# Kernel optimization log

Hardware: AMD Instinct MI355X
Metric: run time of the kernel (lower is better)

## Reference

```python
import jax, jax.numpy as jnp
import numpy as np

CHEB_K = 3

def avwgcn(x, E, W_pool, b_pool):
    # x: [B,N,Cin], E: [N,e], W_pool: [e,K,Cin,Cout], b_pool: [e,Cout]
    N = E.shape[0]
    A = jax.nn.softmax(jax.nn.relu(E @ E.T), axis=1)          # adaptive adjacency [N,N]
    supports = [jnp.eye(N, dtype=x.dtype), A]
    for _ in range(2, CHEB_K):
        supports.append(2.0 * (A @ supports[-1]) - supports[-2])
    S = jnp.stack(supports)                                    # [K,N,N]
    W = jnp.einsum('ne,ekio->nkio', E, W_pool)                 # per-node weights
    b = E @ b_pool                                             # [N,Cout]
    xg = jnp.einsum('knm,bmi->bnki', S, x)                     # Chebyshev graph conv
    return jnp.einsum('bnki,nkio->bno', xg, W) + b


def setup_inputs() -> dict:
    key = jax.random.key(0)
    ks = jax.random.split(key, 7)
    B, N, Din, Dout, E_DIM = 64, 1024, 64, 64, 16
    C = Din + Dout
    return {
        'x': jax.random.normal(ks[0], (B, N, Din), dtype=jnp.float32),
        'state': jax.random.normal(ks[1], (B, N, Dout), dtype=jnp.float32),
        'node_embeddings': jax.random.normal(ks[2], (N, E_DIM), dtype=jnp.float32),
        'gate_W_pool': jax.random.normal(ks[3], (E_DIM, CHEB_K, C, 2 * Dout), dtype=jnp.float32) * 0.1,
        'gate_b_pool': jax.random.normal(ks[4], (E_DIM, 2 * Dout), dtype=jnp.float32) * 0.1,
        'upd_W_pool': jax.random.normal(ks[5], (E_DIM, CHEB_K, C, Dout), dtype=jnp.float32) * 0.1,
        'upd_b_pool': jax.random.normal(ks[6], (E_DIM, Dout), dtype=jnp.float32) * 0.1,
    }


def reference(x, state, node_embeddings, gate_W_pool, gate_b_pool, upd_W_pool, upd_b_pool):
    hidden_dim = state.shape[-1]
    input_and_state = jnp.concatenate([x, state], axis=-1)
    z_r = jax.nn.sigmoid(avwgcn(input_and_state, node_embeddings, gate_W_pool, gate_b_pool))
    z, r = z_r[..., :hidden_dim], z_r[..., hidden_dim:]
    candidate = jnp.concatenate([x, z * state], axis=-1)
    hc = jnp.tanh(avwgcn(candidate, node_embeddings, upd_W_pool, upd_b_pool))
    return r * state + (1.0 - r) * hc
```

## Files before the change

### kernel.cpp

```cpp
#include <hip/hip_runtime.h>
#include <math.h>

#define N_NODES 1024
#define B_SZ 64
#define GNH 4096
#define KI 384
#define EDIM 16
#define WG_NODE 49152
#define WG_WAVE 12288
#define WU_NODE 24576
#define WU_WAVE 6144

typedef _Float16 half8_t __attribute__((ext_vector_type(8)));
typedef float f32x4 __attribute__((ext_vector_type(4)));

__device__ __forceinline__ unsigned short f2h(float f) {
    _Float16 h = (_Float16)f;
    return *(unsigned short*)&h;
}
__device__ __forceinline__ float h2f(unsigned short u) {
    _Float16 h = *(_Float16*)&u;
    return (float)h;
}
__device__ __forceinline__ float sigmoidf_(float v) {
    return 1.f / (1.f + __expf(-v));
}
__device__ __forceinline__ void load_lds16(const void* g, void* l) {
    __builtin_amdgcn_global_load_lds(
        (const __attribute__((address_space(1))) void*)g,
        (__attribute__((address_space(3))) void*)l, 16, 0, 0);
}

__global__ __launch_bounds__(256) void compute_A_kernel(
    const float* __restrict__ E, unsigned short* __restrict__ Ah) {
    __shared__ float red[256];
    const int tid = threadIdx.x;
    const int n = blockIdx.x;
    float en[EDIM];
#pragma unroll
    for (int e = 0; e < EDIM; ++e) en[e] = E[n * EDIM + e];
    float logit[4], lmax = -1e30f;
#pragma unroll
    for (int j = 0; j < 4; ++j) {
        const int m = tid + j * 256;
        float d = 0.f;
#pragma unroll
        for (int e = 0; e < EDIM; ++e) d += en[e] * E[m * EDIM + e];
        d = fmaxf(d, 0.f);
        logit[j] = d;
        lmax = fmaxf(lmax, d);
    }
    red[tid] = lmax;
    __syncthreads();
    for (int s = 128; s > 0; s >>= 1) {
        if (tid < s) red[tid] = fmaxf(red[tid], red[tid + s]);
        __syncthreads();
    }
    lmax = red[0];
    __syncthreads();
    float ex[4], lsum = 0.f;
#pragma unroll
    for (int j = 0; j < 4; ++j) {
        ex[j] = __expf(logit[j] - lmax);
        lsum += ex[j];
    }
    red[tid] = lsum;
    __syncthreads();
    for (int s = 128; s > 0; s >>= 1) {
        if (tid < s) red[tid] += red[tid + s];
        __syncthreads();
    }
    const float inv = 1.f / red[0];
#pragma unroll
    for (int j = 0; j < 4; ++j)
        Ah[n * N_NODES + tid + j * 256] = f2h(ex[j] * inv);
}

__global__ __launch_bounds__(256) void build_T0_all_kernel(
    const float* __restrict__ x, const float* __restrict__ state,
    unsigned short* __restrict__ TX0, unsigned short* __restrict__ TS0,
    unsigned short* __restrict__ TX0T, unsigned short* __restrict__ TS0T) {
    __shared__ unsigned short Lx[64 * 72];
    __shared__ unsigned short Lss[64 * 72];
    const int tid = threadIdx.x;
    const int n0 = blockIdx.x * 64;
    const int b = blockIdx.y;
#pragma unroll
    for (int t = 0; t < 16; ++t) {
        const int id = t * 256 + tid;
        const int nl = id >> 6;
        const int c = id & 63;
        const float xv = x[((size_t)b * N_NODES + n0 + nl) * 64 + c];
        const float sv = state[((size_t)b * N_NODES + n0 + nl) * 64 + c];
        const unsigned short xh = f2h(xv), sh = f2h(sv);
        TX0[(size_t)(n0 + nl) * GNH + b * 64 + c] = xh;
        TS0[(size_t)(n0 + nl) * GNH + b * 64 + c] = sh;
        Lx[c * 72 + nl] = xh;
        Lss[c * 72 + nl] = sh;
    }
    __syncthreads();
#pragma unroll
    for (int t = 0; t < 2; ++t) {
        const int id = t * 256 + tid;
        const int c = id >> 3;
        const int n8 = id & 7;
        uint4 xv = *(const uint4*)&Lx[c * 72 + n8 * 8];
        uint4 sv = *(const uint4*)&Lss[c * 72 + n8 * 8];
        *(uint4*)&TX0T[(size_t)(b * 64 + c) * N_NODES + n0 + n8 * 8] = xv;
        *(uint4*)&TS0T[(size_t)(b * 64 + c) * N_NODES + n0 + n8 * 8] = sv;
    }
}

__global__ __launch_bounds__(256) void transpose16_kernel(
    const unsigned short* __restrict__ src, unsigned short* __restrict__ dst,
    int W) {
    __shared__ unsigned short Ls[64 * 72];
    const int tid = threadIdx.x;
    const int r0 = blockIdx.x * 64;
    const int c0 = blockIdx.y * 64;
#pragma unroll
    for (int t = 0; t < 2; ++t) {
        const int id = t * 256 + tid;
        const int row = id >> 3;
        const int c8 = id & 7;
        uint4 v = *(const uint4*)&src[(size_t)(r0 + row) * W + c0 + c8 * 8];
        const unsigned short* vp = (const unsigned short*)&v;
#pragma unroll
        for (int j = 0; j < 8; ++j) Ls[(c8 * 8 + j) * 72 + row] = vp[j];
    }
    __syncthreads();
#pragma unroll
    for (int t = 0; t < 2; ++t) {
        const int id = t * 256 + tid;
        const int c = id >> 3;
        const int r8 = id & 7;
        uint4 v = *(const uint4*)&Ls[c * 72 + r8 * 8];
        *(uint4*)&dst[(size_t)(c0 + c) * N_NODES + r0 + r8 * 8] = v;
    }
}

__global__ __launch_bounds__(256) void gemm_s2_kernel(
    const unsigned short* __restrict__ Ah,
    const unsigned short* __restrict__ AhT, unsigned short* __restrict__ S2h) {
    __shared__ unsigned short As[64 * 64];
    __shared__ unsigned short Bs[64 * 64];
    const int tid = threadIdx.x;
    const int wave = tid >> 6;
    const int lane = tid & 63;
    const int l15 = lane & 15;
    const int quad = lane >> 4;
    const int n0 = blockIdx.x * 64;
    const int m0 = blockIdx.y * 64;
    const int wn = wave * 16;
    const int lr = lane >> 3;
    const int lsw = (lane & 7) ^ lr;

    f32x4 acc[4] = {};
    for (int k0 = 0; k0 < N_NODES; k0 += 64) {
#pragma unroll
        for (int i = 0; i < 2; ++i) {
            const int rbase = (wave * 2 + i) * 8;
            load_lds16(&Ah[(size_t)(n0 + rbase + lr) * N_NODES + k0 + lsw * 8],
                       &As[rbase * 64]);
            load_lds16(&AhT[(size_t)(m0 + rbase + lr) * N_NODES + k0 + lsw * 8],
                       &Bs[rbase * 64]);
        }
        __syncthreads();
#pragma unroll
        for (int ks = 0; ks < 2; ++ks) {
            const int slot = ((ks * 4 + quad) ^ (l15 & 7)) * 8;
            const half8_t b = *(const half8_t*)&Bs[(wn + l15) * 64 + slot];
#pragma unroll
            for (int mi = 0; mi < 4; ++mi) {
                const half8_t a = *(const half8_t*)&As[(mi * 16 + l15) * 64 + slot];
                acc[mi] =
                    __builtin_amdgcn_mfma_f32_16x16x32_f16(a, b, acc[mi], 0, 0, 0);
            }
        }
        __syncthreads();
    }
#pragma unroll
    for (int mi = 0; mi < 4; ++mi) {
#pragma unroll
        for (int r = 0; r < 4; ++r) {
            const int n_g = n0 + mi * 16 + quad * 4 + r;
            const int m_g = m0 + wn + l15;
            const float v = 2.f * acc[mi][r] - (n_g == m_g ? 1.f : 0.f);
            S2h[(size_t)n_g * N_NODES + m_g] = f2h(v);
        }
    }
}

template <int BM>
__global__ __launch_bounds__(512, 2) void gemm_graph8_kernel(
    const unsigned short* __restrict__ Ah,
    const unsigned short* __restrict__ S2h,
    const unsigned short* __restrict__ BTX,
    const unsigned short* __restrict__ BTS,
    unsigned short* __restrict__ T1X, unsigned short* __restrict__ T1S,
    unsigned short* __restrict__ T2X, unsigned short* __restrict__ T2S,
    int ysplit, int colsPerXcd) {
    constexpr int MFR = BM / 32;
    constexpr int ASLOT_H = BM * 32;
    constexpr int SLOT_H = ASLOT_H + 8192;
    constexpr int APASS = BM / 128;
    constexpr int MT = 2048 / BM;
    __shared__ unsigned short lds[4 * SLOT_H];

    const int tid = threadIdx.x;
    const int wave = tid >> 6;
    const int lane = tid & 63;
    const int l15 = lane & 15;
    const int quad = lane >> 4;
    const int wm = (wave >> 2) * (BM / 2);
    const int wn = (wave & 3) * 64;

    const int id = blockIdx.x;
    const int xcd = id & 7;
    const int j = id >> 3;
    const int mtile = j & (MT - 1);
    const int ytile = xcd * colsPerXcd + j / MT;
    const int mrow0 = mtile * BM;
    const bool isA = mrow0 < N_NODES;
    const unsigned short* Asrc =
        (isA ? Ah : S2h) + (size_t)(mrow0 & 1023) * N_NODES;
    const bool isX = ytile < ysplit;
    const int col0 = (isX ? ytile : ytile - ysplit) * 256;
    const unsigned short* Bsrc = (isX ? BTX : BTS) + (size_t)col0 * N_NODES;
    unsigned short* OUT = (isA ? (isX ? T1X : T1S) : (isX ? T2X : T2S)) +
                          (size_t)(mrow0 & 1023) * GNH + col0;

    int goff[2];
#pragma unroll
    for (int jp = 0; jp < 2; ++jp) {
        const int cell = jp * 512 + tid;
        const int prow = cell >> 3;
        const int q = (cell & 7) ^ (prow & 7);
        goff[jp] = (2 * prow + (q >> 2)) * N_NODES + (q & 3) * 8;
    }

    int offA[MFR], offB[4];
#pragma unroll
    for (int mi = 0; mi < MFR; ++mi) {
        const int prow = (wm >> 1) + mi * 8 + (l15 >> 1);
        const int s8 = ((l15 & 1) * 4 + quad) ^ (prow & 7);
        offA[mi] = prow * 64 + s8 * 8;
    }
#pragma unroll
    for (int ni = 0; ni < 4; ++ni) {
        const int pcol = (wn >> 1) + ni * 8 + (l15 >> 1);
        const int s8 = ((l15 & 1) * 4 + quad) ^ (pcol & 7);
        offB[ni] = ASLOT_H + pcol * 64 + s8 * 8;
    }

    f32x4 acc[MFR][4] = {};

    auto stageA = [&](int t) {
        const int sl = t & 3;
#pragma unroll
        for (int jp = 0; jp < APASS; ++jp)
            load_lds16(Asrc + (size_t)t * 32 + goff[jp],
                       &lds[sl * SLOT_H + jp * 4096 + wave * 512]);
    };
    auto stageB = [&](int t) {
        const int sl = t & 3;
#pragma unroll
        for (int jp = 0; jp < 2; ++jp)
            load_lds16(Bsrc + (size_t)t * 32 + goff[jp],
                       &lds[sl * SLOT_H + ASLOT_H + jp * 4096 + wave * 512]);
    };
    auto waitPipe = [&] {
        if constexpr (BM == 256)
            asm volatile("s_waitcnt vmcnt(8)" ::: "memory");
        else
            asm volatile("s_waitcnt vmcnt(6)" ::: "memory");
    };

    auto tileBody = [&](int t, bool tail) {
        const unsigned short* base = &lds[(t & 3) * SLOT_H];
        half8_t a[MFR], b[4];
#pragma unroll
        for (int mi = 0; mi < MFR; ++mi)
            a[mi] = *(const half8_t*)&base[offA[mi]];
#pragma unroll
        for (int ni = 0; ni < 4; ++ni)
            b[ni] = *(const half8_t*)&base[offB[ni]];
        if (!tail) {
            stageA(t + 3);
            stageB(t + 3);
        }
        __builtin_amdgcn_sched_barrier(0);
        asm volatile("s_waitcnt lgkmcnt(0)" ::: "memory");
        __builtin_amdgcn_sched_barrier(0);
        __builtin_amdgcn_s_setprio(1);
#pragma unroll
        for (int mi = 0; mi < MFR; ++mi)
#pragma unroll
            for (int ni = 0; ni < 4; ++ni)
                acc[mi][ni] = __builtin_amdgcn_mfma_f32_16x16x32_f16(
                    a[mi], b[ni], acc[mi][ni], 0, 0, 0);
        __builtin_amdgcn_s_setprio(0);
        __builtin_amdgcn_sched_barrier(0);
        if (!tail) {
            waitPipe();
        } else {
            asm volatile("s_waitcnt vmcnt(0)" ::: "memory");
        }
        __builtin_amdgcn_sched_barrier(0);
        __builtin_amdgcn_s_barrier();
    };

    stageA(0); stageB(0);
    stageA(1); stageB(1);
    stageA(2); stageB(2);
    waitPipe();
    __builtin_amdgcn_s_barrier();
    __builtin_amdgcn_sched_barrier(0);

#pragma unroll 4
    for (int t = 0; t < 28; ++t) tileBody(t, false);
    tileBody(28, false);
    tileBody(29, true);
    tileBody(30, true);
    tileBody(31, true);

    constexpr int NPASS = BM / 64;
#pragma unroll
    for (int p = 0; p < NPASS; ++p) {
        __syncthreads();
        const int whalf = (BM == 256) ? (p >> 1) : p;
        const int mi0 = (BM == 256) ? (p & 1) * 4 : 0;
        if ((wave >> 2) == whalf) {
#pragma unroll
            for (int mi = 0; mi < 4; ++mi)
#pragma unroll
                for (int ni = 0; ni < 4; ++ni)
#pragma unroll
                    for (int r = 0; r < 4; ++r) {
                        const int row = mi * 16 + quad * 4 + r;
                        const int col = wn + ni * 16 + l15;
                        lds[row * 264 + col] = f2h(acc[mi0 + mi][ni][r]);
                    }
        }
        __syncthreads();
#pragma unroll
        for (int i = 0; i < 4; ++i) {
            const int id2 = i * 512 + tid;
            const int row = id2 >> 5;
            const int c8 = id2 & 31;
            uint4 v = *(const uint4*)&lds[row * 264 + c8 * 8];
            *(uint4*)&OUT[(size_t)(p * 64 + row) * GNH + c8 * 8] = v;
        }
    }
}

__global__ __launch_bounds__(256) void dequant_gate_kernel(
    const float* __restrict__ Wp, const float* __restrict__ E,
    unsigned short* __restrict__ Wt) {
    __shared__ float En[32 * 16];
    const int tid = threadIdx.x;
    const int c8 = blockIdx.x * 256 + tid;
    const int n0 = blockIdx.y * 32;
    const int sub = c8 & 1;
    const int c = c8 >> 1;
    const int l15 = c & 15;
    const int quad = (c >> 4) & 3;
    const int half = (c >> 6) & 1;
    const int ks = (c >> 7) & 3;
    const int sq = c >> 9;
    const int s = sq % 3;
    const int w = sq / 3;
    const int k0 = s * 128 + (ks * 4 + quad) * 8 + sub * 4;
    const int o = w * 32 + half * 16 + l15;

#pragma unroll
    for (int t = 0; t < 2; ++t) {
        const int id = t * 256 + tid;
        En[id] = E[(n0 + (id >> 4)) * EDIM + (id & 15)];
    }
    __syncthreads();

    f32x4 wv[EDIM];
#pragma unroll
    for (int e = 0; e < EDIM; ++e) {
        f32x4 v;
#pragma unroll
        for (int j = 0; j < 4; ++j)
            v[j] = Wp[(size_t)(e * KI + k0 + j) * 128 + o];
        wv[e] = v;
    }

#pragma unroll 4
    for (int nl = 0; nl < 32; ++nl) {
        f32x4 a = {0.f, 0.f, 0.f, 0.f};
#pragma unroll
        for (int e = 0; e < EDIM; ++e) a += wv[e] * En[nl * EDIM + e];
        union { unsigned short u[4]; uint2 v; } pk;
#pragma unroll
        for (int j = 0; j < 4; ++j) pk.u[j] = f2h(a[j]);
        *(uint2*)&Wt[(size_t)(n0 + nl) * WG_NODE + (size_t)c8 * 4] = pk.v;
    }
}

__global__ __launch_bounds__(256) void dequant_upd_kernel(
    const float* __restrict__ Wp, const float* __restrict__ E,
    unsigned short* __restrict__ Wt) {
    __shared__ float En[32 * 16];
    const int tid = threadIdx.x;
    const int c8 = blockIdx.x * 256 + tid;
    const int n0 = blockIdx.y * 32;
    const int sub = c8 & 1;
    const int c = c8 >> 1;
    const int l15 = c & 15;
    const int quad = (c >> 4) & 3;
    const int ks = (c >> 6) & 3;
    const int sq = c >> 8;
    const int s = sq % 3;
    const int w = sq / 3;
    const int k0 = s * 128 + (ks * 4 + quad) * 8 + sub * 4;
    const int o = w * 16 + l15;

#pragma unroll
    for (int t = 0; t < 2; ++t) {
        const int id = t * 256 + tid;
        En[id] = E[(n0 + (id >> 4)) * EDIM + (id & 15)];
    }
    __syncthreads();

    f32x4 wv[EDIM];
#pragma unroll
    for (int e = 0; e < EDIM; ++e) {
        f32x4 v;
#pragma unroll
        for (int j = 0; j < 4; ++j)
            v[j] = Wp[(size_t)(e * KI + k0 + j) * 64 + o];
        wv[e] = v;
    }

#pragma unroll 4
    for (int nl = 0; nl < 32; ++nl) {
        f32x4 a = {0.f, 0.f, 0.f, 0.f};
#pragma unroll
        for (int e = 0; e < EDIM; ++e) a += wv[e] * En[nl * EDIM + e];
        union { unsigned short u[4]; uint2 v; } pk;
#pragma unroll
        for (int j = 0; j < 4; ++j) pk.u[j] = f2h(a[j]);
        *(uint2*)&Wt[(size_t)(n0 + nl) * WU_NODE + (size_t)c8 * 4] = pk.v;
    }
}

__global__ __launch_bounds__(256) void pernode_gate_kernel(
    const unsigned short* __restrict__ TX0,
    const unsigned short* __restrict__ TS0,
    const unsigned short* __restrict__ TX1,
    const unsigned short* __restrict__ TS1,
    const unsigned short* __restrict__ TX2,
    const unsigned short* __restrict__ TS2,
    const unsigned short* __restrict__ Wt, const float* __restrict__ E,
    const float* __restrict__ bp, const float* __restrict__ state,
    unsigned short* __restrict__ rbuf, unsigned short* __restrict__ cand) {
    __shared__ unsigned short XsX[64 * 64];
    __shared__ unsigned short XsS[64 * 64];
    const int n = blockIdx.x;
    const int tid = threadIdx.x;
    const int wave = tid >> 6;
    const int lane = tid & 63;
    const int l15 = lane & 15;
    const int quad = lane >> 4;
    const int wn = wave * 32;
    const int lr = lane >> 3;
    const int lsw = (lane & 7) ^ lr;

    float bias[2];
#pragma unroll
    for (int ni = 0; ni < 2; ++ni) {
        float bv = 0.f;
#pragma unroll
        for (int e = 0; e < EDIM; ++e)
            bv += E[n * EDIM + e] * bp[e * 128 + wn + ni * 16 + l15];
        bias[ni] = bv;
    }

    f32x4 acc[4][2] = {};

    const unsigned short* TXs[3] = {TX0, TX1, TX2};
    const unsigned short* TSs[3] = {TS0, TS1, TS2};
    const unsigned short* wbase =
        Wt + ((size_t)n * 4 + wave) * WG_WAVE + lane * 8;

    for (int s = 0; s < 3; ++s) {
        const unsigned short* xs = TXs[s] + (size_t)n * GNH;
        const unsigned short* ss = TSs[s] + (size_t)n * GNH;
#pragma unroll
        for (int i = 0; i < 2; ++i) {
            const int slab = wave * 2 + i;
            load_lds16(xs + (slab * 8 + lr) * 64 + lsw * 8, &XsX[slab * 512]);
            load_lds16(ss + (slab * 8 + lr) * 64 + lsw * 8, &XsS[slab * 512]);
        }
        __syncthreads();
#pragma unroll
        for (int ks = 0; ks < 4; ++ks) {
            const int kseg = ks * 4 + quad;
            half8_t b[2];
            b[0] = *(const half8_t*)&wbase[((s * 4 + ks) * 2 + 0) * 512];
            b[1] = *(const half8_t*)&wbase[((s * 4 + ks) * 2 + 1) * 512];
            const unsigned short* plane = (kseg < 8) ? XsX : XsS;
            const int aslot = ((kseg & 7) ^ (l15 & 7)) * 8;
#pragma unroll
            for (int mi = 0; mi < 4; ++mi) {
                const half8_t a =
                    *(const half8_t*)&plane[(mi * 16 + l15) * 64 + aslot];
#pragma unroll
                for (int ni = 0; ni < 2; ++ni)
                    acc[mi][ni] = __builtin_amdgcn_mfma_f32_16x16x32_f16(
                        a, b[ni], acc[mi][ni], 0, 0, 0);
            }
        }
        __syncthreads();
    }

#pragma unroll
    for (int mi = 0; mi < 4; ++mi) {
#pragma unroll
        for (int r = 0; r < 4; ++r) {
            const int b_g = mi * 16 + quad * 4 + r;
#pragma unroll
            for (int ni = 0; ni < 2; ++ni) {
                const int o_g = wn + ni * 16 + l15;
                const float v = sigmoidf_(acc[mi][ni][r] + bias[ni]);
                if (o_g < 64) {
                    const float sv =
                        state[((size_t)b_g * N_NODES + n) * 64 + o_g];
                    cand[(size_t)n * GNH + b_g * 64 + o_g] = f2h(v * sv);
                } else {
                    rbuf[((size_t)n * B_SZ + b_g) * 64 + (o_g - 64)] = f2h(v);
                }
            }
        }
    }
}

__global__ __launch_bounds__(256) void pernode_upd_kernel(
    const unsigned short* __restrict__ TX0,
    const unsigned short* __restrict__ CAND,
    const unsigned short* __restrict__ TX1,
    const unsigned short* __restrict__ TS1,
    const unsigned short* __restrict__ TX2,
    const unsigned short* __restrict__ TS2,
    const unsigned short* __restrict__ Wt, const float* __restrict__ E,
    const float* __restrict__ bp, const float* __restrict__ state,
    const unsigned short* __restrict__ rbuf, float* __restrict__ out) {
    __shared__ unsigned short XsX[64 * 64];
    __shared__ unsigned short XsS[64 * 64];
    const int n = blockIdx.x;
    const int tid = threadIdx.x;
    const int wave = tid >> 6;
    const int lane = tid & 63;
    const int l15 = lane & 15;
    const int quad = lane >> 4;
    const int wn = wave * 16;
    const int o_g = wn + l15;
    const int lr = lane >> 3;
    const int lsw = (lane & 7) ^ lr;

    float bias = 0.f;
#pragma unroll
    for (int e = 0; e < EDIM; ++e)
        bias += E[n * EDIM + e] * bp[e * 64 + o_g];

    f32x4 acc[4] = {};

    const unsigned short* TXs[3] = {TX0, TX1, TX2};
    const unsigned short* TSs[3] = {CAND, TS1, TS2};
    const unsigned short* wbase =
        Wt + ((size_t)n * 4 + wave) * WU_WAVE + lane * 8;

    for (int s = 0; s < 3; ++s) {
        const unsigned short* xs = TXs[s] + (size_t)n * GNH;
        const unsigned short* ss = TSs[s] + (size_t)n * GNH;
#pragma unroll
        for (int i = 0; i < 2; ++i) {
            const int slab = wave * 2 + i;
            load_lds16(xs + (slab * 8 + lr) * 64 + lsw * 8, &XsX[slab * 512]);
            load_lds16(ss + (slab * 8 + lr) * 64 + lsw * 8, &XsS[slab * 512]);
        }
        __syncthreads();
#pragma unroll
        for (int ks = 0; ks < 4; ++ks) {
            const int kseg = ks * 4 + quad;
            const half8_t b = *(const half8_t*)&wbase[(s * 4 + ks) * 512];
            const unsigned short* plane = (kseg < 8) ? XsX : XsS;
            const int aslot = ((kseg & 7) ^ (l15 & 7)) * 8;
#pragma unroll
            for (int mi = 0; mi < 4; ++mi) {
                const half8_t a =
                    *(const half8_t*)&plane[(mi * 16 + l15) * 64 + aslot];
                acc[mi] = __builtin_amdgcn_mfma_f32_16x16x32_f16(a, b, acc[mi],
                                                                 0, 0, 0);
            }
        }
        __syncthreads();
    }

#pragma unroll
    for (int mi = 0; mi < 4; ++mi) {
#pragma unroll
        for (int r = 0; r < 4; ++r) {
            const int b_g = mi * 16 + quad * 4 + r;
            const float hc = tanhf(acc[mi][r] + bias);
            const float rr = h2f(rbuf[((size_t)n * B_SZ + b_g) * 64 + o_g]);
            const float sv = state[((size_t)b_g * N_NODES + n) * 64 + o_g];
            out[((size_t)b_g * N_NODES + n) * 64 + o_g] =
                rr * sv + (1.f - rr) * hc;
        }
    }
}

extern "C" void kernel_launch(void* const* d_in, const int* in_sizes, int n_in,
                              void* d_out, int out_size, void* d_ws,
                              size_t ws_size, hipStream_t stream) {
    const float* x = (const float*)d_in[0];
    const float* state = (const float*)d_in[1];
    const float* E = (const float*)d_in[2];
    const float* gW = (const float*)d_in[3];
    const float* gb = (const float*)d_in[4];
    const float* uW = (const float*)d_in[5];
    const float* ub = (const float*)d_in[6];
    float* out = (float*)d_out;

    char* ws = (char*)d_ws;
    unsigned short* Ah = (unsigned short*)ws;
    unsigned short* AhT = (unsigned short*)(ws + 2097152);
    unsigned short* S2h = (unsigned short*)(ws + 4194304);
    unsigned short* TX0 = (unsigned short*)(ws + 6291456);
    unsigned short* TS0 = (unsigned short*)(ws + 14680064);
    unsigned short* TX0T = (unsigned short*)(ws + 23068672);
    unsigned short* TS0T = (unsigned short*)(ws + 31457280);
    unsigned short* TX1 = (unsigned short*)(ws + 39845888);
    unsigned short* TS1 = (unsigned short*)(ws + 48234496);
    unsigned short* TX2 = (unsigned short*)(ws + 56623104);
    unsigned short* TS2 = (unsigned short*)(ws + 65011712);
    unsigned short* Wt = (unsigned short*)(ws + 73400320);
    unsigned short* rbuf = (unsigned short*)(ws + 174063616);
    unsigned short* CAND = (unsigned short*)(ws + 182452224);

    compute_A_kernel<<<N_NODES, 256, 0, stream>>>(E, Ah);
    build_T0_all_kernel<<<dim3(16, 64), 256, 0, stream>>>(x, state, TX0, TS0,
                                                          TX0T, TS0T);
    transpose16_kernel<<<dim3(16, 16), 256, 0, stream>>>(Ah, AhT, N_NODES);
    gemm_s2_kernel<<<dim3(16, 16), 256, 0, stream>>>(Ah, AhT, S2h);

    gemm_graph8_kernel<256><<<256, 512, 0, stream>>>(
        Ah, S2h, TX0T, TS0T, TX1, TS1, TX2, TS2, 16, 4);
    dequant_gate_kernel<<<dim3(48, 32), 256, 0, stream>>>(gW, E, Wt);
    pernode_gate_kernel<<<N_NODES, 256, 0, stream>>>(
        TX0, TS0, TX1, TS1, TX2, TS2, Wt, E, gb, state, rbuf, CAND);
    transpose16_kernel<<<dim3(16, 64), 256, 0, stream>>>(CAND, TS0T, GNH);

    gemm_graph8_kernel<128><<<256, 512, 0, stream>>>(
        Ah, S2h, TX0T, TS0T, TX1, TS1, TX2, TS2, 0, 2);
    dequant_upd_kernel<<<dim3(24, 32), 256, 0, stream>>>(uW, E, Wt);
    pernode_upd_kernel<<<N_NODES, 256, 0, stream>>>(
        TX0, CAND, TX1, TS1, TX2, TS2, Wt, E, ub, state, rbuf, out);
}
```

Measured before the change: 276.1 us.

## Double-buffer MFMA operand fragments in registers across LDS pipeline stages

Tile t+1's A/B fragments are now read from LDS into a second register set while tile t's MFMAs run, using two alternating register buffers. This replaces the old pattern of load fragments, wait lgkmcnt(0), then compute. The intent is to hide LDS read latency behind matrix math. Because fragments for t+2 must now be resident one step earlier, the global-load wait depth is tightened (vmcnt 8→4 and 6→3), which shortens global-prefetch slack and raises register pressure.

```diff
diff --git a/kernel.cpp b/kernel.cpp
--- a/kernel.cpp
+++ b/kernel.cpp
@@ -271,26 +271,26 @@
     };
     auto waitPipe = [&] {
         if constexpr (BM == 256)
-            asm volatile("s_waitcnt vmcnt(8)" ::: "memory");
+            asm volatile("s_waitcnt vmcnt(4)" ::: "memory");
         else
-            asm volatile("s_waitcnt vmcnt(6)" ::: "memory");
+            asm volatile("s_waitcnt vmcnt(3)" ::: "memory");
     };
 
-    auto tileBody = [&](int t, bool tail) {
-        const unsigned short* base = &lds[(t & 3) * SLOT_H];
-        half8_t a[MFR], b[4];
-#pragma unroll
-        for (int mi = 0; mi < MFR; ++mi)
-            a[mi] = *(const half8_t*)&base[offA[mi]];
-#pragma unroll
-        for (int ni = 0; ni < 4; ++ni)
-            b[ni] = *(const half8_t*)&base[offB[ni]];
-        if (!tail) {
+    auto body = [&](int t, half8_t (&aC)[MFR], half8_t (&bC)[4],
+                    half8_t (&aN)[MFR], half8_t (&bN)[4]) {
+        if (t <= 28) {
             stageA(t + 3);
             stageB(t + 3);
         }
-        __builtin_amdgcn_sched_barrier(0);
-        asm volatile("s_waitcnt lgkmcnt(0)" ::: "memory");
+        if (t < 31) {
+            const unsigned short* nbase = &lds[((t + 1) & 3) * SLOT_H];
+#pragma unroll
+            for (int mi = 0; mi < MFR; ++mi)
+                aN[mi] = *(const half8_t*)&nbase[offA[mi]];
+#pragma unroll
+            for (int ni = 0; ni < 4; ++ni)
+                bN[ni] = *(const half8_t*)&nbase[offB[ni]];
+        }
         __builtin_amdgcn_sched_barrier(0);
         __builtin_amdgcn_s_setprio(1);
 #pragma unroll
@@ -298,16 +298,14 @@
 #pragma unroll
             for (int ni = 0; ni < 4; ++ni)
                 acc[mi][ni] = __builtin_amdgcn_mfma_f32_16x16x32_f16(
-                    a[mi], b[ni], acc[mi][ni], 0, 0, 0);
+                    aC[mi], bC[ni], acc[mi][ni], 0, 0, 0);
         __builtin_amdgcn_s_setprio(0);
         __builtin_amdgcn_sched_barrier(0);
-        if (!tail) {
-            waitPipe();
-        } else {
-            asm volatile("s_waitcnt vmcnt(0)" ::: "memory");
-        }
+        if (t < 31) asm volatile("s_waitcnt lgkmcnt(0)" ::: "memory");
+        if (t <= 28) waitPipe();
+        else if (t == 29) asm volatile("s_waitcnt vmcnt(0)" ::: "memory");
         __builtin_amdgcn_sched_barrier(0);
-        __builtin_amdgcn_s_barrier();
+        if (t < 31) __builtin_amdgcn_s_barrier();
     };
 
     stageA(0); stageB(0);
@@ -316,13 +314,27 @@
     waitPipe();
     __builtin_amdgcn_s_barrier();
     __builtin_amdgcn_sched_barrier(0);
-
-#pragma unroll 4
-    for (int t = 0; t < 28; ++t) tileBody(t, false);
-    tileBody(28, false);
-    tileBody(29, true);
-    tileBody(30, true);
-    tileBody(31, true);
+    half8_t aX[MFR], bX[4], aY[MFR], bY[4];
+    {
+        const unsigned short* nbase = &lds[0];
+#pragma unroll
+        for (int mi = 0; mi < MFR; ++mi)
+            aX[mi] = *(const half8_t*)&nbase[offA[mi]];
+#pragma unroll
+        for (int ni = 0; ni < 4; ++ni)
+            bX[ni] = *(const half8_t*)&nbase[offB[ni]];
+    }
+    asm volatile("s_waitcnt lgkmcnt(0)" ::: "memory");
+    __builtin_amdgcn_sched_barrier(0);
+
+    for (int t = 0; t < 28; t += 2) {
+        body(t, aX, bX, aY, bY);
+        body(t + 1, aY, bY, aX, bX);
+    }
+    body(28, aX, bX, aY, bY);
+    body(29, aY, bY, aX, bX);
+    body(30, aX, bX, aY, bY);
+    body(31, aY, bY, aX, bX);
 
     constexpr int NPASS = BM / 64;
 #pragma unroll
```

Result: slower. 283.6 us (+2.7%).

## Use 1024-thread blocks for the BM=256 graph GEMM with 64-row wave tiles

Applied to the files above, without the earlier changes.

The BM=256 graph GEMM instance now launches with 1024 threads (16 waves) instead of 512, so each wave owns a 64x64 output tile (4x4 MFMA fragments) rather than 128x64. The staging loop counts, LDS offsets, vmcnt wait depth and epilogue write-out passes are rederived from the thread count, and the final tile skips its trailing barrier. The aim is to halve the accumulator registers per wave and put more waves on each CU to hide latency, at the cost of larger workgroups and barriers that must synchronise more waves. The BM=128 instance keeps its 512-thread launch but also loses its old launch_bounds(512, 2) occupancy hint.

```diff
diff --git a/kernel.cpp b/kernel.cpp
--- a/kernel.cpp
+++ b/kernel.cpp
@@ -192,7 +192,7 @@
 }
 
 template <int BM>
-__global__ __launch_bounds__(512, 2) void gemm_graph8_kernel(
+__global__ __launch_bounds__(BM * 4) void gemm_graph8_kernel(
     const unsigned short* __restrict__ Ah,
     const unsigned short* __restrict__ S2h,
     const unsigned short* __restrict__ BTX,
@@ -200,11 +200,15 @@
     unsigned short* __restrict__ T1X, unsigned short* __restrict__ T1S,
     unsigned short* __restrict__ T2X, unsigned short* __restrict__ T2S,
     int ysplit, int colsPerXcd) {
-    constexpr int MFR = BM / 32;
+    constexpr int THREADS = BM * 4;
+    constexpr int MFR = 4;
+    constexpr int PWM = 64;
     constexpr int ASLOT_H = BM * 32;
     constexpr int SLOT_H = ASLOT_H + 8192;
-    constexpr int APASS = BM / 128;
+    constexpr int APASS = (BM * 32) / (THREADS * 8);
+    constexpr int BPASS = 8192 / (THREADS * 8);
     constexpr int MT = 2048 / BM;
+    constexpr int ST_I = 2048 / THREADS;
     __shared__ unsigned short lds[4 * SLOT_H];
 
     const int tid = threadIdx.x;
@@ -212,7 +216,7 @@
     const int lane = tid & 63;
     const int l15 = lane & 15;
     const int quad = lane >> 4;
-    const int wm = (wave >> 2) * (BM / 2);
+    const int wm = (wave >> 2) * PWM;
     const int wn = (wave & 3) * 64;
 
     const int id = blockIdx.x;
@@ -230,10 +234,10 @@
     unsigned short* OUT = (isA ? (isX ? T1X : T1S) : (isX ? T2X : T2S)) +
                           (size_t)(mrow0 & 1023) * GNH + col0;
 
-    int goff[2];
-#pragma unroll
-    for (int jp = 0; jp < 2; ++jp) {
-        const int cell = jp * 512 + tid;
+    int goff[BPASS];
+#pragma unroll
+    for (int jp = 0; jp < BPASS; ++jp) {
+        const int cell = jp * THREADS + tid;
         const int prow = cell >> 3;
         const int q = (cell & 7) ^ (prow & 7);
         goff[jp] = (2 * prow + (q >> 2)) * N_NODES + (q & 3) * 8;
@@ -260,18 +264,19 @@
 #pragma unroll
         for (int jp = 0; jp < APASS; ++jp)
             load_lds16(Asrc + (size_t)t * 32 + goff[jp],
-                       &lds[sl * SLOT_H + jp * 4096 + wave * 512]);
+                       &lds[sl * SLOT_H + jp * (THREADS * 8) + wave * 512]);
     };
     auto stageB = [&](int t) {
         const int sl = t & 3;
 #pragma unroll
-        for (int jp = 0; jp < 2; ++jp)
+        for (int jp = 0; jp < BPASS; ++jp)
             load_lds16(Bsrc + (size_t)t * 32 + goff[jp],
-                       &lds[sl * SLOT_H + ASLOT_H + jp * 4096 + wave * 512]);
+                       &lds[sl * SLOT_H + ASLOT_H + jp * (THREADS * 8) +
+                            wave * 512]);
     };
     auto waitPipe = [&] {
         if constexpr (BM == 256)
-            asm volatile("s_waitcnt vmcnt(8)" ::: "memory");
+            asm volatile("s_waitcnt vmcnt(4)" ::: "memory");
         else
             asm volatile("s_waitcnt vmcnt(6)" ::: "memory");
     };
@@ -307,7 +312,7 @@
             asm volatile("s_waitcnt vmcnt(0)" ::: "memory");
         }
         __builtin_amdgcn_sched_barrier(0);
-        __builtin_amdgcn_s_barrier();
+        if (t < 31) __builtin_amdgcn_s_barrier();
     };
 
     stageA(0); stageB(0);
@@ -328,24 +333,22 @@
 #pragma unroll
     for (int p = 0; p < NPASS; ++p) {
         __syncthreads();
-        const int whalf = (BM == 256) ? (p >> 1) : p;
-        const int mi0 = (BM == 256) ? (p & 1) * 4 : 0;
-        if ((wave >> 2) == whalf) {
-#pragma unroll
-            for (int mi = 0; mi < 4; ++mi)
+        if ((wave >> 2) == p) {
+#pragma unroll
+            for (int mi = 0; mi < MFR; ++mi)
 #pragma unroll
                 for (int ni = 0; ni < 4; ++ni)
 #pragma unroll
                     for (int r = 0; r < 4; ++r) {
                         const int row = mi * 16 + quad * 4 + r;
                         const int col = wn + ni * 16 + l15;
-                        lds[row * 264 + col] = f2h(acc[mi0 + mi][ni][r]);
+                        lds[row * 264 + col] = f2h(acc[mi][ni][r]);
                     }
         }
         __syncthreads();
 #pragma unroll
-        for (int i = 0; i < 4; ++i) {
-            const int id2 = i * 512 + tid;
+        for (int i = 0; i < ST_I; ++i) {
+            const int id2 = i * THREADS + tid;
             const int row = id2 >> 5;
             const int c8 = id2 & 31;
             uint4 v = *(const uint4*)&lds[row * 264 + c8 * 8];
@@ -650,7 +653,7 @@
     transpose16_kernel<<<dim3(16, 16), 256, 0, stream>>>(Ah, AhT, N_NODES);
     gemm_s2_kernel<<<dim3(16, 16), 256, 0, stream>>>(Ah, AhT, S2h);
 
-    gemm_graph8_kernel<256><<<256, 512, 0, stream>>>(
+    gemm_graph8_kernel<256><<<256, 1024, 0, stream>>>(
         Ah, S2h, TX0T, TS0T, TX1, TS1, TX2, TS2, 16, 4);
     dequant_gate_kernel<<<dim3(48, 32), 256, 0, stream>>>(gW, E, Wt);
     pernode_gate_kernel<<<N_NODES, 256, 0, stream>>>(
```

New measurement: 278.0 us. Within noise of the previous version (+0.7%).

## Fuse per-node weight dequant into graph GEMM via extra specialized waves

Applied to the files above, without the earlier changes.

Both graph GEMM launches grow from 512 to 768 threads. The extra four waves compute the per-node weight products (E × W_pool → fp16) in lock-step with the GEMM's barriers, which replaces the two standalone dequant kernels. The goal is to drop two launches and hide the dequant work behind the MFMA main loop. The dequant waves follow a barrier count that must match the GEMM path's barrier count exactly. The change also tightens the BM=256 pipeline wait from vmcnt(8) to vmcnt(4), leaves the last tile without its trailing barrier, and drops the two-blocks-per-CU occupancy hint, which may raise register pressure.

```diff
diff --git a/kernel.cpp b/kernel.cpp
--- a/kernel.cpp
+++ b/kernel.cpp
@@ -192,260 +192,231 @@
 }
 
 template <int BM>
-__global__ __launch_bounds__(512, 2) void gemm_graph8_kernel(
+__global__ __launch_bounds__(768) void gemm_graph8_kernel(
     const unsigned short* __restrict__ Ah,
     const unsigned short* __restrict__ S2h,
     const unsigned short* __restrict__ BTX,
     const unsigned short* __restrict__ BTS,
     unsigned short* __restrict__ T1X, unsigned short* __restrict__ T1S,
     unsigned short* __restrict__ T2X, unsigned short* __restrict__ T2S,
-    int ysplit, int colsPerXcd) {
+    const float* __restrict__ Wp, const float* __restrict__ Ef,
+    unsigned short* __restrict__ WtOut, int ysplit, int colsPerXcd) {
     constexpr int MFR = BM / 32;
     constexpr int ASLOT_H = BM * 32;
     constexpr int SLOT_H = ASLOT_H + 8192;
     constexpr int APASS = BM / 128;
     constexpr int MT = 2048 / BM;
+    constexpr int NPASS = BM / 64;
+    constexpr int DQBAR = 1 + 31 + 2 * NPASS;
+    constexpr int NJOBS = (BM == 256) ? 6 : 3;
+    constexpr int IPS = (BM == 256) ? 5 : 3;
+    constexpr int NO_ = (BM == 256) ? 128 : 64;
+    constexpr int WNODE = (BM == 256) ? WG_NODE : WU_NODE;
     __shared__ unsigned short lds[4 * SLOT_H];
 
     const int tid = threadIdx.x;
     const int wave = tid >> 6;
-    const int lane = tid & 63;
-    const int l15 = lane & 15;
-    const int quad = lane >> 4;
-    const int wm = (wave >> 2) * (BM / 2);
-    const int wn = (wave & 3) * 64;
-
-    const int id = blockIdx.x;
-    const int xcd = id & 7;
-    const int j = id >> 3;
-    const int mtile = j & (MT - 1);
-    const int ytile = xcd * colsPerXcd + j / MT;
-    const int mrow0 = mtile * BM;
-    const bool isA = mrow0 < N_NODES;
-    const unsigned short* Asrc =
-        (isA ? Ah : S2h) + (size_t)(mrow0 & 1023) * N_NODES;
-    const bool isX = ytile < ysplit;
-    const int col0 = (isX ? ytile : ytile - ysplit) * 256;
-    const unsigned short* Bsrc = (isX ? BTX : BTS) + (size_t)col0 * N_NODES;
-    unsigned short* OUT = (isA ? (isX ? T1X : T1S) : (isX ? T2X : T2S)) +
-                          (size_t)(mrow0 & 1023) * GNH + col0;
-
-    int goff[2];
-#pragma unroll
-    for (int jp = 0; jp < 2; ++jp) {
-        const int cell = jp * 512 + tid;
-        const int prow = cell >> 3;
-        const int q = (cell & 7) ^ (prow & 7);
-        goff[jp] = (2 * prow + (q >> 2)) * N_NODES + (q & 3) * 8;
-    }
-
-    int offA[MFR], offB[4];
-#pragma unroll
-    for (int mi = 0; mi < MFR; ++mi) {
-        const int prow = (wm >> 1) + mi * 8 + (l15 >> 1);
-        const int s8 = ((l15 & 1) * 4 + quad) ^ (prow & 7);
-        offA[mi] = prow * 64 + s8 * 8;
-    }
-#pragma unroll
-    for (int ni = 0; ni < 4; ++ni) {
-        const int pcol = (wn >> 1) + ni * 8 + (l15 >> 1);
-        const int s8 = ((l15 & 1) * 4 + quad) ^ (pcol & 7);
-        offB[ni] = ASLOT_H + pcol * 64 + s8 * 8;
-    }
-
-    f32x4 acc[MFR][4] = {};
-
-    auto stageA = [&](int t) {
-        const int sl = t & 3;
-#pragma unroll
-        for (int jp = 0; jp < APASS; ++jp)
-            load_lds16(Asrc + (size_t)t * 32 + goff[jp],
-                       &lds[sl * SLOT_H + jp * 4096 + wave * 512]);
-    };
-    auto stageB = [&](int t) {
-        const int sl = t & 3;
-#pragma unroll
-        for (int jp = 0; jp < 2; ++jp)
-            load_lds16(Bsrc + (size_t)t * 32 + goff[jp],
-                       &lds[sl * SLOT_H + ASLOT_H + jp * 4096 + wave * 512]);
-    };
-    auto waitPipe = [&] {
-        if constexpr (BM == 256)
-            asm volatile("s_waitcnt vmcnt(8)" ::: "memory");
-        else
-            asm volatile("s_waitcnt vmcnt(6)" ::: "memory");
-    };
-
-    auto tileBody = [&](int t, bool tail) {
-        const unsigned short* base = &lds[(t & 3) * SLOT_H];
-        half8_t a[MFR], b[4];
-#pragma unroll
-        for (int mi = 0; mi < MFR; ++mi)
-            a[mi] = *(const half8_t*)&base[offA[mi]];
-#pragma unroll
-        for (int ni = 0; ni < 4; ++ni)
-            b[ni] = *(const half8_t*)&base[offB[ni]];
-        if (!tail) {
-            stageA(t + 3);
-            stageB(t + 3);
-        }
+
+    if (wave < 8) {
+        const int lane = tid & 63;
+        const int l15 = lane & 15;
+        const int quad = lane >> 4;
+        const int wm = (wave >> 2) * (BM / 2);
+        const int wn = (wave & 3) * 64;
+
+        const int id = blockIdx.x;
+        const int xcd = id & 7;
+        const int j = id >> 3;
+        const int mtile = j & (MT - 1);
+        const int ytile = xcd * colsPerXcd + j / MT;
+        const int mrow0 = mtile * BM;
+        const bool isA = mrow0 < N_NODES;
+        const unsigned short* Asrc =
+            (isA ? Ah : S2h) + (size_t)(mrow0 & 1023) * N_NODES;
+        const bool isX = ytile < ysplit;
+        const int col0 = (isX ? ytile : ytile - ysplit) * 256;
+        const unsigned short* Bsrc = (isX ? BTX : BTS) + (size_t)col0 * N_NODES;
+        unsigned short* OUT = (isA ? (isX ? T1X : T1S) : (isX ? T2X : T2S)) +
+                              (size_t)(mrow0 & 1023) * GNH + col0;
+
+        int goff[2];
+#pragma unroll
+        for (int jp = 0; jp < 2; ++jp) {
+            const int cell = jp * 512 + tid;
+            const int prow = cell >> 3;
+            const int q = (cell & 7) ^ (prow & 7);
+            goff[jp] = (2 * prow + (q >> 2)) * N_NODES + (q & 3) * 8;
+        }
+
+        int offA[MFR], offB[4];
+#pragma unroll
+        for (int mi = 0; mi < MFR; ++mi) {
+            const int prow = (wm >> 1) + mi * 8 + (l15 >> 1);
+            const int s8 = ((l15 & 1) * 4 + quad) ^ (prow & 7);
+            offA[mi] = prow * 64 + s8 * 8;
+        }
+#pragma unroll
+        for (int ni = 0; ni < 4; ++ni) {
+            const int pcol = (wn >> 1) + ni * 8 + (l15 >> 1);
+            const int s8 = ((l15 & 1) * 4 + quad) ^ (pcol & 7);
+            offB[ni] = ASLOT_H + pcol * 64 + s8 * 8;
+        }
+
+        f32x4 acc[MFR][4] = {};
+
+        auto stageA = [&](int t) {
+            const int sl = t & 3;
+#pragma unroll
+            for (int jp = 0; jp < APASS; ++jp)
+                load_lds16(Asrc + (size_t)t * 32 + goff[jp],
+                           &lds[sl * SLOT_H + jp * 4096 + wave * 512]);
+        };
+        auto stageB = [&](int t) {
+            const int sl = t & 3;
+#pragma unroll
+            for (int jp = 0; jp < 2; ++jp)
+                load_lds16(Bsrc + (size_t)t * 32 + goff[jp],
+                           &lds[sl * SLOT_H + ASLOT_H + jp * 4096 + wave * 512]);
+        };
+        auto waitPipe = [&] {
+            if constexpr (BM == 256)
+                asm volatile("s_waitcnt vmcnt(4)" ::: "memory");
+            else
+                asm volatile("s_waitcnt vmcnt(6)" ::: "memory");
+        };
+
+        auto tileBody = [&](int t, bool tail) {
+            const unsigned short* base = &lds[(t & 3) * SLOT_H];
+            half8_t a[MFR], b[4];
+#pragma unroll
+            for (int mi = 0; mi < MFR; ++mi)
+                a[mi] = *(const half8_t*)&base[offA[mi]];
+#pragma unroll
+            for (int ni = 0; ni < 4; ++ni)
+                b[ni] = *(const half8_t*)&base[offB[ni]];
+            if (!tail) {
+                stageA(t + 3);
+                stageB(t + 3);
+            }
+            __builtin_amdgcn_sched_barrier(0);
+            asm volatile("s_waitcnt lgkmcnt(0)" ::: "memory");
+            __builtin_amdgcn_sched_barrier(0);
+            __builtin_amdgcn_s_setprio(1);
+#pragma unroll
+            for (int mi = 0; mi < MFR; ++mi)
+#pragma unroll
+                for (int ni = 0; ni < 4; ++ni)
+                    acc[mi][ni] = __builtin_amdgcn_mfma_f32_16x16x32_f16(
+                        a[mi], b[ni], acc[mi][ni], 0, 0, 0);
+            __builtin_amdgcn_s_setprio(0);
+            __builtin_amdgcn_sched_barrier(0);
+            if (!tail) {
+                waitPipe();
+            } else {
+                asm volatile("s_waitcnt vmcnt(0)" ::: "memory");
+            }
+            __builtin_amdgcn_sched_barrier(0);
+            if (t < 31) __builtin_amdgcn_s_barrier();
+        };
+
+        stageA(0); stageB(0);
+        stageA(1); stageB(1);
+        stageA(2); stageB(2);
+        waitPipe();
+        __builtin_amdgcn_s_barrier();
         __builtin_amdgcn_sched_barrier(0);
-        asm volatile("s_waitcnt lgkmcnt(0)" ::: "memory");
-        __builtin_amdgcn_sched_barrier(0);
-        __builtin_amdgcn_s_setprio(1);
-#pragma unroll
-        for (int mi = 0; mi < MFR; ++mi)
-#pragma unroll
-            for (int ni = 0; ni < 4; ++ni)
-                acc[mi][ni] = __builtin_amdgcn_mfma_f32_16x16x32_f16(
-                    a[mi], b[ni], acc[mi][ni], 0, 0, 0);
-        __builtin_amdgcn_s_setprio(0);
-        __builtin_amdgcn_sched_barrier(0);
-        if (!tail) {
-            waitPipe();
-        } else {
-            asm volatile("s_waitcnt vmcnt(0)" ::: "memory");
-        }
-        __builtin_amdgcn_sched_barrier(0);
-        __builtin_amdgcn_s_barrier();
-    };
-
-    stageA(0); stageB(0);
-    stageA(1); stageB(1);
-    stageA(2); stageB(2);
-    waitPipe();
-    __builtin_amdgcn_s_barrier();
-    __builtin_amdgcn_sched_barrier(0);
 
 #pragma unroll 4
-    for (int t = 0; t < 28; ++t) tileBody(t, false);
-    tileBody(28, false);
-    tileBody(29, true);
-    tileBody(30, true);
-    tileBody(31, true);
-
-    constexpr int NPASS = BM / 64;
-#pragma unroll
-    for (int p = 0; p < NPASS; ++p) {
-        __syncthreads();
-        const int whalf = (BM == 256) ? (p >> 1) : p;
-        const int mi0 = (BM == 256) ? (p & 1) * 4 : 0;
-        if ((wave >> 2) == whalf) {
-#pragma unroll
-            for (int mi = 0; mi < 4; ++mi)
-#pragma unroll
-                for (int ni = 0; ni < 4; ++ni)
-#pragma unroll
-                    for (int r = 0; r < 4; ++r) {
-                        const int row = mi * 16 + quad * 4 + r;
-                        const int col = wn + ni * 16 + l15;
-                        lds[row * 264 + col] = f2h(acc[mi0 + mi][ni][r]);
+        for (int t = 0; t < 28; ++t) tileBody(t, false);
+        tileBody(28, false);
+        tileBody(29, true);
+        tileBody(30, true);
+        tileBody(31, true);
+
+#pragma unroll
+        for (int p = 0; p < NPASS; ++p) {
+            __syncthreads();
+            const int whalf = (BM == 256) ? (p >> 1) : p;
+            const int mi0 = (BM == 256) ? (p & 1) * 4 : 0;
+            if ((wave >> 2) == whalf) {
+#pragma unroll
+                for (int mi = 0; mi < 4; ++mi)
+#pragma unroll
+                    for (int ni = 0; ni < 4; ++ni)
+#pragma unroll
+                        for (int r = 0; r < 4; ++r) {
+                            const int row = mi * 16 + quad * 4 + r;
+                            const int col = wn + ni * 16 + l15;
+                            lds[row * 264 + col] = f2h(acc[mi0 + mi][ni][r]);
+                        }
+            }
+            __syncthreads();
+#pragma unroll
+            for (int i = 0; i < 4; ++i) {
+                const int id2 = i * 512 + tid;
+                const int row = id2 >> 5;
+                const int c8 = id2 & 31;
+                uint4 v = *(const uint4*)&lds[row * 264 + c8 * 8];
+                *(uint4*)&OUT[(size_t)(p * 64 + row) * GNH + c8 * 8] = v;
+            }
+        }
+    } else {
+        const int dqt = tid - 512;
+        const int g = blockIdx.x >> 3;
+        const int slice = blockIdx.x & 7;
+        const int n0 = g * 32;
+        f32x4 wv[EDIM];
+        int job = 0, node = 32;
+        int c8cur = 0;
+        for (int slot = 0; slot < DQBAR; ++slot) {
+            for (int q = 0; q < IPS; ++q) {
+                if (node == 32 && job < NJOBS) {
+                    c8cur = slice * (NJOBS * 256) + job * 256 + dqt;
+                    const int sub = c8cur & 1;
+                    const int c = c8cur >> 1;
+                    const int l15v = c & 15;
+                    const int quadv = (c >> 4) & 3;
+                    int k0, o;
+                    if (BM == 256) {
+                        const int halfv = (c >> 6) & 1;
+                        const int ksv = (c >> 7) & 3;
+                        const int sq = c >> 9;
+                        k0 = (sq % 3) * 128 + (ksv * 4 + quadv) * 8 + sub * 4;
+                        o = (sq / 3) * 32 + halfv * 16 + l15v;
+                    } else {
+                        const int ksv = (c >> 6) & 3;
+                        const int sq = c >> 8;
+                        k0 = (sq % 3) * 128 + (ksv * 4 + quadv) * 8 + sub * 4;
+                        o = (sq / 3) * 16 + l15v;
                     }
-        }
-        __syncthreads();
-#pragma unroll
-        for (int i = 0; i < 4; ++i) {
-            const int id2 = i * 512 + tid;
-            const int row = id2 >> 5;
-            const int c8 = id2 & 31;
-            uint4 v = *(const uint4*)&lds[row * 264 + c8 * 8];
-            *(uint4*)&OUT[(size_t)(p * 64 + row) * GNH + c8 * 8] = v;
-        }
-    }
-}
-
-__global__ __launch_bounds__(256) void dequant_gate_kernel(
-    const float* __restrict__ Wp, const float* __restrict__ E,
-    unsigned short* __restrict__ Wt) {
-    __shared__ float En[32 * 16];
-    const int tid = threadIdx.x;
-    const int c8 = blockIdx.x * 256 + tid;
-    const int n0 = blockIdx.y * 32;
-    const int sub = c8 & 1;
-    const int c = c8 >> 1;
-    const int l15 = c & 15;
-    const int quad = (c >> 4) & 3;
-    const int half = (c >> 6) & 1;
-    const int ks = (c >> 7) & 3;
-    const int sq = c >> 9;
-    const int s = sq % 3;
-    const int w = sq / 3;
-    const int k0 = s * 128 + (ks * 4 + quad) * 8 + sub * 4;
-    const int o = w * 32 + half * 16 + l15;
-
-#pragma unroll
-    for (int t = 0; t < 2; ++t) {
-        const int id = t * 256 + tid;
-        En[id] = E[(n0 + (id >> 4)) * EDIM + (id & 15)];
-    }
-    __syncthreads();
-
-    f32x4 wv[EDIM];
-#pragma unroll
-    for (int e = 0; e < EDIM; ++e) {
-        f32x4 v;
-#pragma unroll
-        for (int j = 0; j < 4; ++j)
-            v[j] = Wp[(size_t)(e * KI + k0 + j) * 128 + o];
-        wv[e] = v;
-    }
-
-#pragma unroll 4
-    for (int nl = 0; nl < 32; ++nl) {
-        f32x4 a = {0.f, 0.f, 0.f, 0.f};
-#pragma unroll
-        for (int e = 0; e < EDIM; ++e) a += wv[e] * En[nl * EDIM + e];
-        union { unsigned short u[4]; uint2 v; } pk;
-#pragma unroll
-        for (int j = 0; j < 4; ++j) pk.u[j] = f2h(a[j]);
-        *(uint2*)&Wt[(size_t)(n0 + nl) * WG_NODE + (size_t)c8 * 4] = pk.v;
-    }
-}
-
-__global__ __launch_bounds__(256) void dequant_upd_kernel(
-    const float* __restrict__ Wp, const float* __restrict__ E,
-    unsigned short* __restrict__ Wt) {
-    __shared__ float En[32 * 16];
-    const int tid = threadIdx.x;
-    const int c8 = blockIdx.x * 256 + tid;
-    const int n0 = blockIdx.y * 32;
-    const int sub = c8 & 1;
-    const int c = c8 >> 1;
-    const int l15 = c & 15;
-    const int quad = (c >> 4) & 3;
-    const int ks = (c >> 6) & 3;
-    const int sq = c >> 8;
-    const int s = sq % 3;
-    const int w = sq / 3;
-    const int k0 = s * 128 + (ks * 4 + quad) * 8 + sub * 4;
-    const int o = w * 16 + l15;
-
-#pragma unroll
-    for (int t = 0; t < 2; ++t) {
-        const int id = t * 256 + tid;
-        En[id] = E[(n0 + (id >> 4)) * EDIM + (id & 15)];
-    }
-    __syncthreads();
-
-    f32x4 wv[EDIM];
-#pragma unroll
-    for (int e = 0; e < EDIM; ++e) {
-        f32x4 v;
-#pragma unroll
-        for (int j = 0; j < 4; ++j)
-            v[j] = Wp[(size_t)(e * KI + k0 + j) * 64 + o];
-        wv[e] = v;
-    }
-
-#pragma unroll 4
-    for (int nl = 0; nl < 32; ++nl) {
-        f32x4 a = {0.f, 0.f, 0.f, 0.f};
-#pragma unroll
-        for (int e = 0; e < EDIM; ++e) a += wv[e] * En[nl * EDIM + e];
-        union { unsigned short u[4]; uint2 v; } pk;
-#pragma unroll
-        for (int j = 0; j < 4; ++j) pk.u[j] = f2h(a[j]);
-        *(uint2*)&Wt[(size_t)(n0 + nl) * WU_NODE + (size_t)c8 * 4] = pk.v;
+#pragma unroll
+                    for (int e = 0; e < EDIM; ++e) {
+                        f32x4 v;
+#pragma unroll
+                        for (int jj = 0; jj < 4; ++jj)
+                            v[jj] = Wp[(size_t)(e * KI + k0 + jj) * NO_ + o];
+                        wv[e] = v;
+                    }
+                    node = 0;
+                    ++job;
+                }
+                if (node < 32) {
+                    f32x4 a = {0.f, 0.f, 0.f, 0.f};
+#pragma unroll
+                    for (int e = 0; e < EDIM; ++e)
+                        a += wv[e] * Ef[(size_t)(n0 + node) * EDIM + e];
+                    union { unsigned short u[4]; uint2 v2; } pk;
+#pragma unroll
+                    for (int jj = 0; jj < 4; ++jj) pk.u[jj] = f2h(a[jj]);
+                    *(uint2*)&WtOut[(size_t)(n0 + node) * WNODE +
+                                    (size_t)c8cur * 4] = pk.v2;
+                    ++node;
+                }
+            }
+            __builtin_amdgcn_sched_barrier(0);
+            __builtin_amdgcn_s_barrier();
+            __builtin_amdgcn_sched_barrier(0);
+        }
     }
 }
 
@@ -650,16 +621,14 @@
     transpose16_kernel<<<dim3(16, 16), 256, 0, stream>>>(Ah, AhT, N_NODES);
     gemm_s2_kernel<<<dim3(16, 16), 256, 0, stream>>>(Ah, AhT, S2h);
 
-    gemm_graph8_kernel<256><<<256, 512, 0, stream>>>(
-        Ah, S2h, TX0T, TS0T, TX1, TS1, TX2, TS2, 16, 4);
-    dequant_gate_kernel<<<dim3(48, 32), 256, 0, stream>>>(gW, E, Wt);
+    gemm_graph8_kernel<256><<<256, 768, 0, stream>>>(
+        Ah, S2h, TX0T, TS0T, TX1, TS1, TX2, TS2, gW, E, Wt, 16, 4);
     pernode_gate_kernel<<<N_NODES, 256, 0, stream>>>(
         TX0, TS0, TX1, TS1, TX2, TS2, Wt, E, gb, state, rbuf, CAND);
     transpose16_kernel<<<dim3(16, 64), 256, 0, stream>>>(CAND, TS0T, GNH);
 
-    gemm_graph8_kernel<128><<<256, 512, 0, stream>>>(
-        Ah, S2h, TX0T, TS0T, TX1, TS1, TX2, TS2, 0, 2);
-    dequant_upd_kernel<<<dim3(24, 32), 256, 0, stream>>>(uW, E, Wt);
+    gemm_graph8_kernel<128><<<256, 768, 0, stream>>>(
+        Ah, S2h, TX0T, TS0T, TX1, TS1, TX2, TS2, uW, E, Wt, 0, 2);
     pernode_upd_kernel<<<N_NODES, 256, 0, stream>>>(
         TX0, CAND, TX1, TS1, TX2, TS2, Wt, E, ub, state, rbuf, out);
 }
```

After: 424.1 us. 1.54x slower.
